# Performance work log

Measured on AMD Instinct MI355X. Metric: run time of the kernel, lower is better.

The kernel has to match this reference:

```python
import jax, jax.numpy as jnp
import numpy as np

B, S, D = 4, 2048, 1024
H = 16
HD = D // H  # head dim = 64


def setup_inputs() -> dict:
    key = jax.random.key(0)
    ks = jax.random.split(key, 9)
    s = 1.0 / np.sqrt(D)
    return {
        "Q": jax.random.normal(ks[0], (B, S, D), dtype=jnp.float32),
        "K": jax.random.normal(ks[1], (B, S, D), dtype=jnp.float32),
        "V": jax.random.normal(ks[2], (B, S, D), dtype=jnp.float32),
        "Wq": jax.random.uniform(ks[3], (D, D), jnp.float32, -s, s),
        "bq": jax.random.uniform(ks[4], (D,), jnp.float32, -s, s),
        "Wk": jax.random.uniform(ks[5], (D, D), jnp.float32, -s, s),
        "bk": jax.random.uniform(ks[6], (D,), jnp.float32, -s, s),
        "Wv": jax.random.uniform(ks[7], (D, D), jnp.float32, -s, s),
        "bv": jax.random.uniform(ks[8], (D,), jnp.float32, -s, s),
    }


def reference(Q, K, V, Wq, bq, Wk, bk, Wv, bv):
    # Linear projections, split into heads: (B, H, S, HD)
    def proj(x, W, b):
        y = x @ W + b  # torch Linear uses x @ W.T; here W is stored pre-transposed (D_in, D_out)
        return y.reshape(B, S, H, HD).transpose(0, 2, 1, 3)

    q = proj(Q, Wq, bq)
    k = proj(K, Wk, bk)
    v = proj(V, Wv, bv)

    scale = 1.0 / jnp.sqrt(jnp.float32(HD))
    scores = jnp.einsum("bhqd,bhkd->bhqk", q, k) * scale  # (B,H,S,S)
    # causal mask (mask=True path): -inf above the diagonal
    causal = jnp.triu(jnp.full((S, S), -jnp.inf, dtype=scores.dtype), k=1)
    scores = scores + causal
    attn = jax.nn.softmax(scores, axis=-1)
    ctx = jnp.einsum("bhqk,bhkd->bhqd", attn, v)  # (B,H,S,HD)
    return ctx.transpose(0, 2, 1, 3).reshape(B, S, H * HD)
```

## Files before the change

### kernel.cpp

```cpp
#include <hip/hip_runtime.h>
#include <hip/hip_bf16.h>
#include <stdint.h>

#define B_  4
#define S_  2048
#define D_  1024
#define H_  16
#define HD_ 64
#define LOG2E 1.44269504088896f

typedef unsigned short u16;
typedef short bf16x8 __attribute__((ext_vector_type(8)));
typedef float f32x4 __attribute__((ext_vector_type(4)));

static __device__ __forceinline__ u16 f2bf(float f) {
    union { float f; uint32_t u; } v; v.f = f;
    return (u16)((v.u + 0x7FFF + ((v.u >> 16) & 1)) >> 16);
}

static __device__ __forceinline__ uint32_t cvt_pk_bf16(float lo, float hi) {
    uint32_t r;
    asm("v_cvt_pk_bf16_f32 %0, %1, %2" : "=v"(r) : "v"(lo), "v"(hi));
    return r;
}

static __device__ __forceinline__ uint32_t pk2(float lo, float hi) {
    return __builtin_amdgcn_perm(__float_as_uint(hi), __float_as_uint(lo), 0x07060302u);
}

static __device__ __forceinline__ bf16x8 rd_swz(const u16* base, int row, int slot) {
    return *(const bf16x8*)((const char*)base + row * 128 + ((slot ^ (row & 7)) << 4));
}

static __device__ __forceinline__ void gll_swz(const u16* grow0, size_t stride,
                                               u16* lds_chunk, int lane) {
    const int r = lane >> 3;
    const int slot = (lane & 7) ^ r;
    const u16* g = grow0 + (size_t)r * stride + slot * 8;
    __builtin_amdgcn_global_load_lds(
        (const __attribute__((address_space(1))) uint32_t*)g,
        (__attribute__((address_space(3))) uint32_t*)lds_chunk, 16, 0, 0);
}

__global__ __launch_bounds__(256) void wtrans(
    const float* __restrict__ W0, const float* __restrict__ W1, const float* __restrict__ W2,
    u16* __restrict__ T0, u16* __restrict__ T1, u16* __restrict__ T2)
{
    const float* W = blockIdx.z == 0 ? W0 : (blockIdx.z == 1 ? W1 : W2);
    u16* T       = blockIdx.z == 0 ? T0 : (blockIdx.z == 1 ? T1 : T2);
    __shared__ float t[32][33];
    const int n0 = blockIdx.x * 32, k0 = blockIdx.y * 32;
    const int tx = threadIdx.x, ty = threadIdx.y;
#pragma unroll
    for (int i = 0; i < 4; ++i)
        t[ty + i * 8][tx] = W[(size_t)(k0 + ty + i * 8) * D_ + n0 + tx];
    __syncthreads();
#pragma unroll
    for (int i = 0; i < 4; ++i)
        T[(size_t)(n0 + ty + i * 8) * D_ + k0 + tx] = f2bf(t[tx][ty + i * 8]);
}

template <int MODE>
__global__ __launch_bounds__(256) void proj_gemm(
    const float* __restrict__ X, const u16* __restrict__ Wt,
    const float* __restrict__ bias, u16* __restrict__ out)
{
    __shared__ __align__(16) u16 lA[2][128 * 64];
    __shared__ __align__(16) u16 lB[2][128 * 64];
    const int tid = threadIdx.x;
    const int m0 = blockIdx.x * 128, n0 = blockIdx.y * 128;
    const int w = tid >> 6, lane = tid & 63;
    const int lr = lane & 15, lg = lane >> 4;
    const int wr = (w >> 1) * 64, wc = (w & 1) * 64;

    f32x4 acc[4][4] = {};
    float4 areg[8];

    auto loadA = [&](int k0) {
#pragma unroll
        for (int i = 0; i < 8; ++i) {
            const int lin = i * 1024 + tid * 4;
            const int r = lin >> 6, c = lin & 63;
            areg[i] = *(const float4*)(X + (size_t)(m0 + r) * D_ + k0 + c);
        }
    };
    auto writeA = [&](u16* dst) {
#pragma unroll
        for (int i = 0; i < 8; ++i) {
            const int lin = i * 1024 + tid * 4;
            const int r = lin >> 6, c = lin & 63;
            uint2 pk;
            pk.x = pk2(areg[i].x, areg[i].y);
            pk.y = pk2(areg[i].z, areg[i].w);
            const int phys = r * 128 + (((c >> 3) ^ (r & 7)) << 4) + ((c & 7) << 1);
            *(uint2*)((char*)dst + phys) = pk;
        }
    };
    auto stageB = [&](int k0, u16* dst) {
#pragma unroll
        for (int i = 0; i < 4; ++i) {
            const int c = w * 4 + i;
            gll_swz(Wt + (size_t)(n0 + c * 8) * D_ + k0, D_, dst + c * 512, lane);
        }
    };
    auto mfmaStep = [&](const u16* A, const u16* Bb) {
#pragma unroll
        for (int kk = 0; kk < 2; ++kk) {
            bf16x8 af[4], bfr[4];
#pragma unroll
            for (int m = 0; m < 4; ++m)
                af[m] = rd_swz(A, wr + m * 16 + lr, kk * 4 + lg);
#pragma unroll
            for (int n = 0; n < 4; ++n)
                bfr[n] = rd_swz(Bb, wc + n * 16 + lr, kk * 4 + lg);
#pragma unroll
            for (int m = 0; m < 4; ++m)
#pragma unroll
                for (int n = 0; n < 4; ++n)
                    acc[m][n] = __builtin_amdgcn_mfma_f32_16x16x32_bf16(af[m], bfr[n], acc[m][n], 0, 0, 0);
        }
    };

    loadA(0);
    stageB(0, lB[0]);
    writeA(lA[0]);
    __syncthreads();

    for (int k0 = 0, s = 0; k0 < D_; k0 += 64, s ^= 1) {
        const int nk = k0 + 64;
        if (nk < D_) {
            loadA(nk);
            stageB(nk, lB[s ^ 1]);
        }
        mfmaStep(lA[s], lB[s]);
        if (nk < D_) writeA(lA[s ^ 1]);
        __syncthreads();
    }

#pragma unroll
    for (int m = 0; m < 4; ++m)
#pragma unroll
        for (int n = 0; n < 4; ++n)
#pragma unroll
            for (int j = 0; j < 4; ++j) {
                const int gm = m0 + wr + m * 16 + lg * 4 + j;
                const int gn = n0 + wc + n * 16 + lr;
                float y = acc[m][n][j] + bias[gn];
                if (MODE == 0) y *= 0.125f * LOG2E;
                const int bb = gm >> 11, s2 = gm & (S_ - 1);
                const int h = gn >> 6, hd = gn & 63;
                size_t off;
                if (MODE < 2) off = (((size_t)bb * H_ + h) * S_ + s2) * HD_ + hd;
                else {
                    const int s6 = s2 & 63;
                    const int sp = (s2 & ~63) | (s6 & 0x20) | ((s6 & 0xC) << 1) |
                                   ((s6 & 0x10) >> 2) | (s6 & 3);
                    off = (((size_t)bb * H_ + h) * HD_ + hd) * S_ + sp;
                }
                out[off] = f2bf(y);
            }
}

__global__ __launch_bounds__(512) void attn_kernel(
    const u16* __restrict__ qb, const u16* __restrict__ kb,
    const u16* __restrict__ vtb, float* __restrict__ out)
{
    const int bh = blockIdx.y;
    const int b = bh >> 4, h = bh & 15;
    const int tid = threadIdx.x;
    const int w = tid >> 6, lane = tid & 63;
    const int lr = lane & 15, lg = lane >> 4;

    __shared__ __align__(16) u16 lds[2][4][64 * 64];

    const size_t kbase = (size_t)bh * S_ * HD_;
    const size_t vbase = (size_t)bh * HD_ * S_;

    union { uint32_t u[4]; bf16x8 v; } onesf;
    onesf.u[0] = onesf.u[1] = onesf.u[2] = onesf.u[3] = 0x3F803F80u;

    for (int e = 0; e < 2; ++e) {
        const int qi = (e == 0) ? (int)blockIdx.x : 15 - (int)blockIdx.x;
        const int q0 = qi * 128;
        const int qrow = q0 + w * 16 + lr;

        const size_t qoff = ((size_t)bh * S_ + qrow) * HD_;
        const bf16x8 qf0 = *(const bf16x8*)(qb + qoff + lg * 8);
        const bf16x8 qf1 = *(const bf16x8*)(qb + qoff + 32 + lg * 8);

        f32x4 oacc[4] = {};
        f32x4 lacc = {};

        const int tmax = 2 * qi + 1;

        auto stage = [&](int tp, int s) {
            const int kvA = tp * 64, kvB = kvA + 64;
            u16* d = &lds[s][0][0];
            gll_swz(kb + kbase + (size_t)(kvA + w * 8) * HD_, HD_, d + w * 512, lane);
            gll_swz(vtb + vbase + (size_t)(w * 8) * S_ + kvA, S_, d + 4096 + w * 512, lane);
            gll_swz(kb + kbase + (size_t)(kvB + w * 8) * HD_, HD_, d + 8192 + w * 512, lane);
            gll_swz(vtb + vbase + (size_t)(w * 8) * S_ + kvB, S_, d + 12288 + w * 512, lane);
        };

        auto compute = [&](int t, const u16* lK, const u16* lV) {
            const int kv0 = t * 64;
            f32x4 sacc[4];
            __builtin_amdgcn_s_setprio(1);
#pragma unroll
            for (int n = 0; n < 4; ++n) {
                const bf16x8 k0f = rd_swz(lK, n * 16 + lr, lg);
                const bf16x8 k1f = rd_swz(lK, n * 16 + lr, 4 + lg);
                f32x4 z = {};
                z = __builtin_amdgcn_mfma_f32_16x16x32_bf16(k0f, qf0, z, 0, 0, 0);
                z = __builtin_amdgcn_mfma_f32_16x16x32_bf16(k1f, qf1, z, 0, 0, 0);
                sacc[n] = z;
            }
            __builtin_amdgcn_s_setprio(0);

            if (t >= tmax - 1) {
#pragma unroll
                for (int n = 0; n < 4; ++n)
#pragma unroll
                    for (int j = 0; j < 4; ++j)
                        if (kv0 + n * 16 + lg * 4 + j > qrow) sacc[n][j] = -1e30f;
            }

            uint32_t pw[4][2];
#pragma unroll
            for (int n = 0; n < 4; ++n)
#pragma unroll
                for (int jh = 0; jh < 2; ++jh)
                    pw[n][jh] = cvt_pk_bf16(exp2f(sacc[n][2 * jh]),
                                            exp2f(sacc[n][2 * jh + 1]));

            union { uint32_t u[4]; bf16x8 v; } a0, a1;
            a0.u[0] = pw[0][0]; a0.u[1] = pw[0][1];
            a0.u[2] = pw[1][0]; a0.u[3] = pw[1][1];
            a1.u[0] = pw[2][0]; a1.u[1] = pw[2][1];
            a1.u[2] = pw[3][0]; a1.u[3] = pw[3][1];

            __builtin_amdgcn_s_setprio(1);
#pragma unroll
            for (int n = 0; n < 4; ++n) {
                const int row = n * 16 + lr;
                const bf16x8 vf0 = rd_swz(lV, row, lg);
                const bf16x8 vf1 = rd_swz(lV, row, 4 + lg);
                oacc[n] = __builtin_amdgcn_mfma_f32_16x16x32_bf16(a0.v, vf0, oacc[n], 0, 0, 0);
                oacc[n] = __builtin_amdgcn_mfma_f32_16x16x32_bf16(a1.v, vf1, oacc[n], 0, 0, 0);
            }
            lacc = __builtin_amdgcn_mfma_f32_16x16x32_bf16(a0.v, onesf.v, lacc, 0, 0, 0);
            lacc = __builtin_amdgcn_mfma_f32_16x16x32_bf16(a1.v, onesf.v, lacc, 0, 0, 0);
            __builtin_amdgcn_s_setprio(0);
        };

        stage(0, 0);
        __syncthreads();

        for (int tp = 0, s = 0; tp <= tmax; tp += 2, s ^= 1) {
            if (tp + 2 <= tmax) stage(tp + 2, s ^ 1);
            const u16* base = &lds[s][0][0];
            compute(tp, base, base + 4096);
            if (!(tp + 1 == tmax && w < 4)) compute(tp + 1, base + 8192, base + 12288);
            __syncthreads();
        }

        f32x4 inv;
#pragma unroll
        for (int j = 0; j < 4; ++j) inv[j] = 1.f / lacc[j];
#pragma unroll
        for (int j = 0; j < 4; ++j) {
            const int row = q0 + w * 16 + lg * 4 + j;
#pragma unroll
            for (int n = 0; n < 4; ++n)
                out[((size_t)b * S_ + row) * D_ + h * HD_ + n * 16 + lr] = oacc[n][j] * inv[j];
        }
    }
}

extern "C" void kernel_launch(void* const* d_in, const int* in_sizes, int n_in,
                              void* d_out, int out_size, void* d_ws, size_t ws_size,
                              hipStream_t stream) {
    const float* Q  = (const float*)d_in[0];
    const float* K  = (const float*)d_in[1];
    const float* V  = (const float*)d_in[2];
    const float* Wq = (const float*)d_in[3];
    const float* bq = (const float*)d_in[4];
    const float* Wk = (const float*)d_in[5];
    const float* bk = (const float*)d_in[6];
    const float* Wv = (const float*)d_in[7];
    const float* bv = (const float*)d_in[8];
    float* out = (float*)d_out;

    char* ws = (char*)d_ws;
    const size_t WT_BYTES  = (size_t)D_ * D_ * 2;
    const size_t QKV_BYTES = (size_t)B_ * S_ * D_ * 2;
    u16* Wtq = (u16*)(ws);
    u16* Wtk = (u16*)(ws + WT_BYTES);
    u16* Wtv = (u16*)(ws + 2 * WT_BYTES);
    u16* qb  = (u16*)(ws + 3 * WT_BYTES);
    u16* kb  = (u16*)(ws + 3 * WT_BYTES + QKV_BYTES);
    u16* vtb = (u16*)(ws + 3 * WT_BYTES + 2 * QKV_BYTES);

    wtrans<<<dim3(32, 32, 3), dim3(32, 8), 0, stream>>>(Wq, Wk, Wv, Wtq, Wtk, Wtv);
    proj_gemm<0><<<dim3(64, 8), dim3(256), 0, stream>>>(Q, Wtq, bq, qb);
    proj_gemm<1><<<dim3(64, 8), dim3(256), 0, stream>>>(K, Wtk, bk, kb);
    proj_gemm<2><<<dim3(64, 8), dim3(256), 0, stream>>>(V, Wtv, bv, vtb);
    attn_kernel<<<dim3(8, B_ * H_), dim3(512), 0, stream>>>(qb, kb, vtb, out);
}
```

Before: 150.8 us.

## Merge QKV projections into one launch and reschedule attention blocks per query tile

The three projection GEMMs become one launch indexed by blockIdx.z, which removes two kernel launches and lets the three GEMMs fill the GPU together. The attention kernel no longer has each block process a paired query tile (qi and 15-qi). It now launches 1024 blocks, each handling one query tile, with a permutation table that spreads causal work across slots and rounds. LDS double buffering is replaced by a single buffer loaded synchronously, which lowers LDS use so more blocks can be resident, at the cost of no longer overlapping loads with compute.

```diff
diff --git a/kernel.cpp b/kernel.cpp
--- a/kernel.cpp
+++ b/kernel.cpp
@@ -60,11 +60,18 @@
         T[(size_t)(n0 + ty + i * 8) * D_ + k0 + tx] = f2bf(t[tx][ty + i * 8]);
 }
 
-template <int MODE>
-__global__ __launch_bounds__(256) void proj_gemm(
-    const float* __restrict__ X, const u16* __restrict__ Wt,
-    const float* __restrict__ bias, u16* __restrict__ out)
+__global__ __launch_bounds__(256) void proj_fused(
+    const float* __restrict__ Xq, const float* __restrict__ Xk, const float* __restrict__ Xv,
+    const u16* __restrict__ Wtq, const u16* __restrict__ Wtk, const u16* __restrict__ Wtv,
+    const float* __restrict__ bq, const float* __restrict__ bk, const float* __restrict__ bv,
+    u16* __restrict__ oq, u16* __restrict__ ok, u16* __restrict__ ov)
 {
+    const int mode = blockIdx.z;
+    const float* X   = mode == 0 ? Xq : (mode == 1 ? Xk : Xv);
+    const u16*  Wt   = mode == 0 ? Wtq : (mode == 1 ? Wtk : Wtv);
+    const float* bias = mode == 0 ? bq : (mode == 1 ? bk : bv);
+    u16* out         = mode == 0 ? oq : (mode == 1 ? ok : ov);
+
     __shared__ __align__(16) u16 lA[2][128 * 64];
     __shared__ __align__(16) u16 lB[2][128 * 64];
     const int tid = threadIdx.x;
@@ -146,11 +153,11 @@
                 const int gm = m0 + wr + m * 16 + lg * 4 + j;
                 const int gn = n0 + wc + n * 16 + lr;
                 float y = acc[m][n][j] + bias[gn];
-                if (MODE == 0) y *= 0.125f * LOG2E;
+                if (mode == 0) y *= 0.125f * LOG2E;
                 const int bb = gm >> 11, s2 = gm & (S_ - 1);
                 const int h = gn >> 6, hd = gn & 63;
                 size_t off;
-                if (MODE < 2) off = (((size_t)bb * H_ + h) * S_ + s2) * HD_ + hd;
+                if (mode < 2) off = (((size_t)bb * H_ + h) * S_ + s2) * HD_ + hd;
                 else {
                     const int s6 = s2 & 63;
                     const int sp = (s2 & ~63) | (s6 & 0x20) | ((s6 & 0xC) << 1) |
@@ -165,13 +172,17 @@
     const u16* __restrict__ qb, const u16* __restrict__ kb,
     const u16* __restrict__ vtb, float* __restrict__ out)
 {
-    const int bh = blockIdx.y;
+    const int bid = blockIdx.x;
+    const int slot = bid & 255, round = bid >> 8;
+    const int s15 = slot & 15;
+    const int qi = (int)((0x4B3C691E5A2D780FULL >> (((s15 ^ round) & 15) * 4)) & 15);
+    const int bh = (round << 4) | (slot >> 4);
     const int b = bh >> 4, h = bh & 15;
     const int tid = threadIdx.x;
     const int w = tid >> 6, lane = tid & 63;
     const int lr = lane & 15, lg = lane >> 4;
 
-    __shared__ __align__(16) u16 lds[2][4][64 * 64];
+    __shared__ __align__(16) u16 lds4[4][64 * 64];
 
     const size_t kbase = (size_t)bh * S_ * HD_;
     const size_t vbase = (size_t)bh * HD_ * S_;
@@ -179,101 +190,90 @@
     union { uint32_t u[4]; bf16x8 v; } onesf;
     onesf.u[0] = onesf.u[1] = onesf.u[2] = onesf.u[3] = 0x3F803F80u;
 
-    for (int e = 0; e < 2; ++e) {
-        const int qi = (e == 0) ? (int)blockIdx.x : 15 - (int)blockIdx.x;
-        const int q0 = qi * 128;
-        const int qrow = q0 + w * 16 + lr;
-
-        const size_t qoff = ((size_t)bh * S_ + qrow) * HD_;
-        const bf16x8 qf0 = *(const bf16x8*)(qb + qoff + lg * 8);
-        const bf16x8 qf1 = *(const bf16x8*)(qb + qoff + 32 + lg * 8);
-
-        f32x4 oacc[4] = {};
-        f32x4 lacc = {};
-
-        const int tmax = 2 * qi + 1;
-
-        auto stage = [&](int tp, int s) {
-            const int kvA = tp * 64, kvB = kvA + 64;
-            u16* d = &lds[s][0][0];
-            gll_swz(kb + kbase + (size_t)(kvA + w * 8) * HD_, HD_, d + w * 512, lane);
-            gll_swz(vtb + vbase + (size_t)(w * 8) * S_ + kvA, S_, d + 4096 + w * 512, lane);
-            gll_swz(kb + kbase + (size_t)(kvB + w * 8) * HD_, HD_, d + 8192 + w * 512, lane);
-            gll_swz(vtb + vbase + (size_t)(w * 8) * S_ + kvB, S_, d + 12288 + w * 512, lane);
-        };
-
-        auto compute = [&](int t, const u16* lK, const u16* lV) {
-            const int kv0 = t * 64;
-            f32x4 sacc[4];
-            __builtin_amdgcn_s_setprio(1);
-#pragma unroll
-            for (int n = 0; n < 4; ++n) {
-                const bf16x8 k0f = rd_swz(lK, n * 16 + lr, lg);
-                const bf16x8 k1f = rd_swz(lK, n * 16 + lr, 4 + lg);
-                f32x4 z = {};
-                z = __builtin_amdgcn_mfma_f32_16x16x32_bf16(k0f, qf0, z, 0, 0, 0);
-                z = __builtin_amdgcn_mfma_f32_16x16x32_bf16(k1f, qf1, z, 0, 0, 0);
-                sacc[n] = z;
-            }
-            __builtin_amdgcn_s_setprio(0);
-
-            if (t >= tmax - 1) {
-#pragma unroll
-                for (int n = 0; n < 4; ++n)
-#pragma unroll
-                    for (int j = 0; j < 4; ++j)
-                        if (kv0 + n * 16 + lg * 4 + j > qrow) sacc[n][j] = -1e30f;
-            }
-
-            uint32_t pw[4][2];
+    const int q0 = qi * 128;
+    const int qrow = q0 + w * 16 + lr;
+    const size_t qoff = ((size_t)bh * S_ + qrow) * HD_;
+    const bf16x8 qf0 = *(const bf16x8*)(qb + qoff + lg * 8);
+    const bf16x8 qf1 = *(const bf16x8*)(qb + qoff + 32 + lg * 8);
+
+    f32x4 oacc[4] = {};
+    f32x4 lacc = {};
+
+    const int tmax = 2 * qi + 1;
+
+    auto compute = [&](int t, const u16* lK, const u16* lV) {
+        const int kv0 = t * 64;
+        f32x4 sacc[4];
+        __builtin_amdgcn_s_setprio(1);
+#pragma unroll
+        for (int n = 0; n < 4; ++n) {
+            const bf16x8 k0f = rd_swz(lK, n * 16 + lr, lg);
+            const bf16x8 k1f = rd_swz(lK, n * 16 + lr, 4 + lg);
+            f32x4 z = {};
+            z = __builtin_amdgcn_mfma_f32_16x16x32_bf16(k0f, qf0, z, 0, 0, 0);
+            z = __builtin_amdgcn_mfma_f32_16x16x32_bf16(k1f, qf1, z, 0, 0, 0);
+            sacc[n] = z;
+        }
+        __builtin_amdgcn_s_setprio(0);
+
+        if (t >= tmax - 1) {
 #pragma unroll
             for (int n = 0; n < 4; ++n)
 #pragma unroll
-                for (int jh = 0; jh < 2; ++jh)
-                    pw[n][jh] = cvt_pk_bf16(exp2f(sacc[n][2 * jh]),
-                                            exp2f(sacc[n][2 * jh + 1]));
-
-            union { uint32_t u[4]; bf16x8 v; } a0, a1;
-            a0.u[0] = pw[0][0]; a0.u[1] = pw[0][1];
-            a0.u[2] = pw[1][0]; a0.u[3] = pw[1][1];
-            a1.u[0] = pw[2][0]; a1.u[1] = pw[2][1];
-            a1.u[2] = pw[3][0]; a1.u[3] = pw[3][1];
-
-            __builtin_amdgcn_s_setprio(1);
-#pragma unroll
-            for (int n = 0; n < 4; ++n) {
-                const int row = n * 16 + lr;
-                const bf16x8 vf0 = rd_swz(lV, row, lg);
-                const bf16x8 vf1 = rd_swz(lV, row, 4 + lg);
-                oacc[n] = __builtin_amdgcn_mfma_f32_16x16x32_bf16(a0.v, vf0, oacc[n], 0, 0, 0);
-                oacc[n] = __builtin_amdgcn_mfma_f32_16x16x32_bf16(a1.v, vf1, oacc[n], 0, 0, 0);
-            }
-            lacc = __builtin_amdgcn_mfma_f32_16x16x32_bf16(a0.v, onesf.v, lacc, 0, 0, 0);
-            lacc = __builtin_amdgcn_mfma_f32_16x16x32_bf16(a1.v, onesf.v, lacc, 0, 0, 0);
-            __builtin_amdgcn_s_setprio(0);
-        };
-
-        stage(0, 0);
+                for (int j = 0; j < 4; ++j)
+                    if (kv0 + n * 16 + lg * 4 + j > qrow) sacc[n][j] = -1e30f;
+        }
+
+        uint32_t pw[4][2];
+#pragma unroll
+        for (int n = 0; n < 4; ++n)
+#pragma unroll
+            for (int jh = 0; jh < 2; ++jh)
+                pw[n][jh] = cvt_pk_bf16(exp2f(sacc[n][2 * jh]),
+                                        exp2f(sacc[n][2 * jh + 1]));
+
+        union { uint32_t u[4]; bf16x8 v; } a0, a1;
+        a0.u[0] = pw[0][0]; a0.u[1] = pw[0][1];
+        a0.u[2] = pw[1][0]; a0.u[3] = pw[1][1];
+        a1.u[0] = pw[2][0]; a1.u[1] = pw[2][1];
+        a1.u[2] = pw[3][0]; a1.u[3] = pw[3][1];
+
+        __builtin_amdgcn_s_setprio(1);
+#pragma unroll
+        for (int n = 0; n < 4; ++n) {
+            const int row = n * 16 + lr;
+            const bf16x8 vf0 = rd_swz(lV, row, lg);
+            const bf16x8 vf1 = rd_swz(lV, row, 4 + lg);
+            oacc[n] = __builtin_amdgcn_mfma_f32_16x16x32_bf16(a0.v, vf0, oacc[n], 0, 0, 0);
+            oacc[n] = __builtin_amdgcn_mfma_f32_16x16x32_bf16(a1.v, vf1, oacc[n], 0, 0, 0);
+        }
+        lacc = __builtin_amdgcn_mfma_f32_16x16x32_bf16(a0.v, onesf.v, lacc, 0, 0, 0);
+        lacc = __builtin_amdgcn_mfma_f32_16x16x32_bf16(a1.v, onesf.v, lacc, 0, 0, 0);
+        __builtin_amdgcn_s_setprio(0);
+    };
+
+    for (int tp = 0; tp <= tmax; tp += 2) {
+        const int kvA = tp * 64, kvB = kvA + 64;
         __syncthreads();
-
-        for (int tp = 0, s = 0; tp <= tmax; tp += 2, s ^= 1) {
-            if (tp + 2 <= tmax) stage(tp + 2, s ^ 1);
-            const u16* base = &lds[s][0][0];
-            compute(tp, base, base + 4096);
-            if (!(tp + 1 == tmax && w < 4)) compute(tp + 1, base + 8192, base + 12288);
-            __syncthreads();
-        }
-
-        f32x4 inv;
-#pragma unroll
-        for (int j = 0; j < 4; ++j) inv[j] = 1.f / lacc[j];
-#pragma unroll
-        for (int j = 0; j < 4; ++j) {
-            const int row = q0 + w * 16 + lg * 4 + j;
-#pragma unroll
-            for (int n = 0; n < 4; ++n)
-                out[((size_t)b * S_ + row) * D_ + h * HD_ + n * 16 + lr] = oacc[n][j] * inv[j];
-        }
+        gll_swz(kb + kbase + (size_t)(kvA + w * 8) * HD_, HD_, &lds4[0][w * 512], lane);
+        gll_swz(vtb + vbase + (size_t)(w * 8) * S_ + kvA, S_, &lds4[1][w * 512], lane);
+        gll_swz(kb + kbase + (size_t)(kvB + w * 8) * HD_, HD_, &lds4[2][w * 512], lane);
+        gll_swz(vtb + vbase + (size_t)(w * 8) * S_ + kvB, S_, &lds4[3][w * 512], lane);
+        __syncthreads();
+
+        compute(tp, lds4[0], lds4[1]);
+        if (!(tp + 1 == tmax && w < 4)) compute(tp + 1, lds4[2], lds4[3]);
+    }
+
+    f32x4 inv;
+#pragma unroll
+    for (int j = 0; j < 4; ++j) inv[j] = 1.f / lacc[j];
+#pragma unroll
+    for (int j = 0; j < 4; ++j) {
+        const int row = q0 + w * 16 + lg * 4 + j;
+#pragma unroll
+        for (int n = 0; n < 4; ++n)
+            out[((size_t)b * S_ + row) * D_ + h * HD_ + n * 16 + lr] = oacc[n][j] * inv[j];
     }
 }
 
@@ -302,8 +302,7 @@
     u16* vtb = (u16*)(ws + 3 * WT_BYTES + 2 * QKV_BYTES);
 
     wtrans<<<dim3(32, 32, 3), dim3(32, 8), 0, stream>>>(Wq, Wk, Wv, Wtq, Wtk, Wtv);
-    proj_gemm<0><<<dim3(64, 8), dim3(256), 0, stream>>>(Q, Wtq, bq, qb);
-    proj_gemm<1><<<dim3(64, 8), dim3(256), 0, stream>>>(K, Wtk, bk, kb);
-    proj_gemm<2><<<dim3(64, 8), dim3(256), 0, stream>>>(V, Wtv, bv, vtb);
-    attn_kernel<<<dim3(8, B_ * H_), dim3(512), 0, stream>>>(qb, kb, vtb, out);
-}
+    proj_fused<<<dim3(64, 8, 3), dim3(256), 0, stream>>>(Q, K, V, Wtq, Wtk, Wtv,
+                                                         bq, bk, bv, qb, kb, vtb);
+    attn_kernel<<<dim3(1024), dim3(512), 0, stream>>>(qb, kb, vtb, out);
+}
```

Result: slower. 161.3 us (+6.9%).

## Process two 16-row query slices per wave to reuse K/V LDS tiles

Applied to the files above, without the earlier changes.

Each wave now handles 32 query rows, split into two 16-row sub-tiles, so every K/V fragment read from LDS feeds twice as many MFMAs. Each block covers 256 queries and the grid becomes 256 one-dimensional blocks, with bh in the low bits and a causal pair index in the high bits. Tiles lying fully above the diagonal are skipped per wave, and the first sub-tile is skipped per tile when it is fully masked. The aim is to cut LDS traffic per FLOP. The cost is fewer blocks (256 instead of 512), more register pressure from the doubled accumulators, and coarser causal load balancing.

```diff
diff --git a/kernel.cpp b/kernel.cpp
--- a/kernel.cpp
+++ b/kernel.cpp
@@ -165,7 +165,9 @@
     const u16* __restrict__ qb, const u16* __restrict__ kb,
     const u16* __restrict__ vtb, float* __restrict__ out)
 {
-    const int bh = blockIdx.y;
+    const int bx = blockIdx.x;
+    const int bh = bx & 63;
+    const int pi = bx >> 6;
     const int b = bh >> 4, h = bh & 15;
     const int tid = threadIdx.x;
     const int w = tid >> 6, lane = tid & 63;
@@ -180,22 +182,25 @@
     onesf.u[0] = onesf.u[1] = onesf.u[2] = onesf.u[3] = 0x3F803F80u;
 
     for (int e = 0; e < 2; ++e) {
-        const int qi = (e == 0) ? (int)blockIdx.x : 15 - (int)blockIdx.x;
-        const int q0 = qi * 128;
-        const int qrow = q0 + w * 16 + lr;
-
-        const size_t qoff = ((size_t)bh * S_ + qrow) * HD_;
-        const bf16x8 qf0 = *(const bf16x8*)(qb + qoff + lg * 8);
-        const bf16x8 qf1 = *(const bf16x8*)(qb + qoff + 32 + lg * 8);
-
-        f32x4 oacc[4] = {};
-        f32x4 lacc = {};
-
-        const int tmax = 2 * qi + 1;
-
-        auto stage = [&](int tp, int s) {
+        const int qi = e ? (7 - pi) : pi;
+        const int q0 = qi * 256;
+        const int qrb = q0 + w * 32;
+
+        bf16x8 qf0[2], qf1[2];
+#pragma unroll
+        for (int s = 0; s < 2; ++s) {
+            const size_t qoff = ((size_t)bh * S_ + qrb + s * 16 + lr) * HD_;
+            qf0[s] = *(const bf16x8*)(qb + qoff + lg * 8);
+            qf1[s] = *(const bf16x8*)(qb + qoff + 32 + lg * 8);
+        }
+
+        f32x4 oacc[2][4] = {};
+        f32x4 lacc[2] = {};
+        const int tmax = 4 * qi + 3;
+
+        auto stage = [&](int tp, int set) {
             const int kvA = tp * 64, kvB = kvA + 64;
-            u16* d = &lds[s][0][0];
+            u16* d = &lds[set][0][0];
             gll_swz(kb + kbase + (size_t)(kvA + w * 8) * HD_, HD_, d + w * 512, lane);
             gll_swz(vtb + vbase + (size_t)(w * 8) * S_ + kvA, S_, d + 4096 + w * 512, lane);
             gll_swz(kb + kbase + (size_t)(kvB + w * 8) * HD_, HD_, d + 8192 + w * 512, lane);
@@ -204,40 +209,55 @@
 
         auto compute = [&](int t, const u16* lK, const u16* lV) {
             const int kv0 = t * 64;
-            f32x4 sacc[4];
+            if (kv0 > qrb + 31) return;
+            const bool a0 = (kv0 <= qrb + 15);
+
+            f32x4 sacc[2][4];
             __builtin_amdgcn_s_setprio(1);
 #pragma unroll
             for (int n = 0; n < 4; ++n) {
                 const bf16x8 k0f = rd_swz(lK, n * 16 + lr, lg);
                 const bf16x8 k1f = rd_swz(lK, n * 16 + lr, 4 + lg);
-                f32x4 z = {};
-                z = __builtin_amdgcn_mfma_f32_16x16x32_bf16(k0f, qf0, z, 0, 0, 0);
-                z = __builtin_amdgcn_mfma_f32_16x16x32_bf16(k1f, qf1, z, 0, 0, 0);
-                sacc[n] = z;
+                f32x4 z1 = {};
+                z1 = __builtin_amdgcn_mfma_f32_16x16x32_bf16(k0f, qf0[1], z1, 0, 0, 0);
+                z1 = __builtin_amdgcn_mfma_f32_16x16x32_bf16(k1f, qf1[1], z1, 0, 0, 0);
+                sacc[1][n] = z1;
+                if (a0) {
+                    f32x4 z0 = {};
+                    z0 = __builtin_amdgcn_mfma_f32_16x16x32_bf16(k0f, qf0[0], z0, 0, 0, 0);
+                    z0 = __builtin_amdgcn_mfma_f32_16x16x32_bf16(k1f, qf1[0], z0, 0, 0, 0);
+                    sacc[0][n] = z0;
+                }
             }
             __builtin_amdgcn_s_setprio(0);
 
-            if (t >= tmax - 1) {
+            if (t >= tmax - 3) {
+#pragma unroll
+                for (int s = 0; s < 2; ++s)
+#pragma unroll
+                    for (int n = 0; n < 4; ++n)
+#pragma unroll
+                        for (int j = 0; j < 4; ++j)
+                            if (kv0 + n * 16 + lg * 4 + j > qrb + s * 16 + lr)
+                                sacc[s][n][j] = -1e30f;
+            }
+
+            union { uint32_t u[4]; bf16x8 v; } pa[2][2];
+#pragma unroll
+            for (int s = 0; s < 2; ++s) {
+                if (s == 0 && !a0) continue;
+                uint32_t pw[4][2];
 #pragma unroll
                 for (int n = 0; n < 4; ++n)
 #pragma unroll
-                    for (int j = 0; j < 4; ++j)
-                        if (kv0 + n * 16 + lg * 4 + j > qrow) sacc[n][j] = -1e30f;
-            }
-
-            uint32_t pw[4][2];
-#pragma unroll
-            for (int n = 0; n < 4; ++n)
-#pragma unroll
-                for (int jh = 0; jh < 2; ++jh)
-                    pw[n][jh] = cvt_pk_bf16(exp2f(sacc[n][2 * jh]),
-                                            exp2f(sacc[n][2 * jh + 1]));
-
-            union { uint32_t u[4]; bf16x8 v; } a0, a1;
-            a0.u[0] = pw[0][0]; a0.u[1] = pw[0][1];
-            a0.u[2] = pw[1][0]; a0.u[3] = pw[1][1];
-            a1.u[0] = pw[2][0]; a1.u[1] = pw[2][1];
-            a1.u[2] = pw[3][0]; a1.u[3] = pw[3][1];
+                    for (int jh = 0; jh < 2; ++jh)
+                        pw[n][jh] = cvt_pk_bf16(exp2f(sacc[s][n][2 * jh]),
+                                                exp2f(sacc[s][n][2 * jh + 1]));
+                pa[s][0].u[0] = pw[0][0]; pa[s][0].u[1] = pw[0][1];
+                pa[s][0].u[2] = pw[1][0]; pa[s][0].u[3] = pw[1][1];
+                pa[s][1].u[0] = pw[2][0]; pa[s][1].u[1] = pw[2][1];
+                pa[s][1].u[2] = pw[3][0]; pa[s][1].u[3] = pw[3][1];
+            }
 
             __builtin_amdgcn_s_setprio(1);
 #pragma unroll
@@ -245,34 +265,45 @@
                 const int row = n * 16 + lr;
                 const bf16x8 vf0 = rd_swz(lV, row, lg);
                 const bf16x8 vf1 = rd_swz(lV, row, 4 + lg);
-                oacc[n] = __builtin_amdgcn_mfma_f32_16x16x32_bf16(a0.v, vf0, oacc[n], 0, 0, 0);
-                oacc[n] = __builtin_amdgcn_mfma_f32_16x16x32_bf16(a1.v, vf1, oacc[n], 0, 0, 0);
-            }
-            lacc = __builtin_amdgcn_mfma_f32_16x16x32_bf16(a0.v, onesf.v, lacc, 0, 0, 0);
-            lacc = __builtin_amdgcn_mfma_f32_16x16x32_bf16(a1.v, onesf.v, lacc, 0, 0, 0);
+                oacc[1][n] = __builtin_amdgcn_mfma_f32_16x16x32_bf16(pa[1][0].v, vf0, oacc[1][n], 0, 0, 0);
+                oacc[1][n] = __builtin_amdgcn_mfma_f32_16x16x32_bf16(pa[1][1].v, vf1, oacc[1][n], 0, 0, 0);
+                if (a0) {
+                    oacc[0][n] = __builtin_amdgcn_mfma_f32_16x16x32_bf16(pa[0][0].v, vf0, oacc[0][n], 0, 0, 0);
+                    oacc[0][n] = __builtin_amdgcn_mfma_f32_16x16x32_bf16(pa[0][1].v, vf1, oacc[0][n], 0, 0, 0);
+                }
+            }
+            lacc[1] = __builtin_amdgcn_mfma_f32_16x16x32_bf16(pa[1][0].v, onesf.v, lacc[1], 0, 0, 0);
+            lacc[1] = __builtin_amdgcn_mfma_f32_16x16x32_bf16(pa[1][1].v, onesf.v, lacc[1], 0, 0, 0);
+            if (a0) {
+                lacc[0] = __builtin_amdgcn_mfma_f32_16x16x32_bf16(pa[0][0].v, onesf.v, lacc[0], 0, 0, 0);
+                lacc[0] = __builtin_amdgcn_mfma_f32_16x16x32_bf16(pa[0][1].v, onesf.v, lacc[0], 0, 0, 0);
+            }
             __builtin_amdgcn_s_setprio(0);
         };
 
         stage(0, 0);
         __syncthreads();
 
-        for (int tp = 0, s = 0; tp <= tmax; tp += 2, s ^= 1) {
-            if (tp + 2 <= tmax) stage(tp + 2, s ^ 1);
-            const u16* base = &lds[s][0][0];
-            compute(tp, base, base + 4096);
-            if (!(tp + 1 == tmax && w < 4)) compute(tp + 1, base + 8192, base + 12288);
+        for (int tp = 0, st = 0; tp <= tmax; tp += 2, st ^= 1) {
+            if (tp + 2 <= tmax) stage(tp + 2, st ^ 1);
+            const u16* d = &lds[st][0][0];
+            compute(tp, d, d + 4096);
+            compute(tp + 1, d + 8192, d + 12288);
             __syncthreads();
         }
 
-        f32x4 inv;
-#pragma unroll
-        for (int j = 0; j < 4; ++j) inv[j] = 1.f / lacc[j];
-#pragma unroll
-        for (int j = 0; j < 4; ++j) {
-            const int row = q0 + w * 16 + lg * 4 + j;
-#pragma unroll
-            for (int n = 0; n < 4; ++n)
-                out[((size_t)b * S_ + row) * D_ + h * HD_ + n * 16 + lr] = oacc[n][j] * inv[j];
+#pragma unroll
+        for (int s = 0; s < 2; ++s) {
+            f32x4 inv;
+#pragma unroll
+            for (int j = 0; j < 4; ++j) inv[j] = 1.f / lacc[s][j];
+#pragma unroll
+            for (int j = 0; j < 4; ++j) {
+                const int row = q0 + w * 32 + s * 16 + lg * 4 + j;
+#pragma unroll
+                for (int n = 0; n < 4; ++n)
+                    out[((size_t)b * S_ + row) * D_ + h * HD_ + n * 16 + lr] = oacc[s][n][j] * inv[j];
+            }
         }
     }
 }
@@ -305,5 +336,5 @@
     proj_gemm<0><<<dim3(64, 8), dim3(256), 0, stream>>>(Q, Wtq, bq, qb);
     proj_gemm<1><<<dim3(64, 8), dim3(256), 0, stream>>>(K, Wtk, bk, kb);
     proj_gemm<2><<<dim3(64, 8), dim3(256), 0, stream>>>(V, Wtv, bv, vtb);
-    attn_kernel<<<dim3(8, B_ * H_), dim3(512), 0, stream>>>(qb, kb, vtb, out);
-}
+    attn_kernel<<<dim3(256), dim3(512), 0, stream>>>(qb, kb, vtb, out);
+}
```

After: 151.6 us. Within noise of the previous version (+0.5%).
